# Performance work log

Hardware: AMD Instinct MI355X
Metric: run time of the kernel (lower is better)

Reference implementation:

```python
import jax, jax.numpy as jnp
import numpy as np

N = 100000
E = 1600000
IN_C = 128
OUT_C = 64
EDGE_DIM = 16
EDGE_HID = 32
EPS = 1e-5


def setup_inputs() -> dict:
    key = jax.random.key(0)
    ks = jax.random.split(key, 12)
    x = jax.random.normal(ks[0], (N, IN_C), dtype=jnp.float32)
    edge_index = jax.random.randint(ks[1], (2, E), 0, N, dtype=jnp.int64)
    edge_attr = jax.random.uniform(ks[2], (E, EDGE_DIM), dtype=jnp.float32)
    # PDNConv params
    lin_w = jax.random.normal(ks[3], (OUT_C, IN_C), dtype=jnp.float32) / np.sqrt(IN_C)
    bias = jnp.zeros((OUT_C,), dtype=jnp.float32)
    mlp_w1 = jax.random.normal(ks[4], (EDGE_HID, EDGE_DIM), dtype=jnp.float32) / np.sqrt(EDGE_DIM)
    mlp_b1 = jnp.zeros((EDGE_HID,), dtype=jnp.float32)
    mlp_w2 = jax.random.normal(ks[5], (1, EDGE_HID), dtype=jnp.float32) / np.sqrt(EDGE_HID)
    mlp_b2 = jnp.zeros((1,), dtype=jnp.float32)
    # PReLU (single shared parameter, torch default init 0.25)
    prelu_a = jnp.asarray(0.25, dtype=jnp.float32)
    # GraphNorm params
    gn_weight = jnp.ones((OUT_C,), dtype=jnp.float32)
    gn_bias = jnp.zeros((OUT_C,), dtype=jnp.float32)
    gn_mean_scale = jnp.ones((OUT_C,), dtype=jnp.float32)
    return {
        "x": x, "edge_index": edge_index, "edge_attr": edge_attr,
        "lin_w": lin_w, "bias": bias,
        "mlp_w1": mlp_w1, "mlp_b1": mlp_b1, "mlp_w2": mlp_w2, "mlp_b2": mlp_b2,
        "prelu_a": prelu_a,
        "gn_weight": gn_weight, "gn_bias": gn_bias, "gn_mean_scale": gn_mean_scale,
    }


def reference(x, edge_index, edge_attr, lin_w, bias, mlp_w1, mlp_b1, mlp_w2, mlp_b2,
              prelu_a, gn_weight, gn_bias, gn_mean_scale):
    n = x.shape[0]
    # --- PDNConv ---
    # edge MLP: Linear -> ReLU -> Linear -> Sigmoid -> scalar gate per edge
    h = jax.nn.relu(edge_attr @ mlp_w1.T + mlp_b1)           # [E, hid]
    ew = jax.nn.sigmoid(h @ mlp_w2.T + mlp_b2)[:, 0]         # [E]
    # add self-loops with weight 1.0
    loop = jnp.arange(n)
    row = jnp.concatenate([edge_index[0], loop])             # source
    col = jnp.concatenate([edge_index[1], loop])             # target
    ew = jnp.concatenate([ew, jnp.ones((n,), dtype=x.dtype)])
    # gcn_norm: D^{-1/2} A D^{-1/2} with weighted degree on targets
    deg = jax.ops.segment_sum(ew, col, num_segments=n)       # [N]
    dinv = jnp.where(deg > 0, jax.lax.rsqrt(deg), 0.0)
    norm = dinv[row] * ew * dinv[col]                        # [E+N]
    xt = x @ lin_w.T                                         # [N, out]
    msgs = norm[:, None] * xt[row]                           # gather + gate
    out = jax.ops.segment_sum(msgs, col, num_segments=n) + bias  # scatter-add
    # --- PReLU ---
    out = jnp.where(out >= 0, out, prelu_a * out)
    # --- GraphNorm (single graph) ---
    mean = out.mean(axis=0)                                  # [out]
    centered = out - gn_mean_scale * mean
    var = jnp.mean(centered * centered, axis=0)
    out = gn_weight * centered * jax.lax.rsqrt(var + EPS) + gn_bias
    return out
```

## Files before the change

kernel.cpp:

```cpp
#include <hip/hip_runtime.h>
#include <math.h>

#define IN_C   128
#define OUT_C  64
#define EDIM   16
#define EHID   32
#define GN_EPS 1e-5f

typedef unsigned long long u64;

__device__ __forceinline__ float dot4(float4 a, float4 b) {
    return a.x * b.x + a.y * b.y + a.z * b.z + a.w * b.w;
}
__device__ __forceinline__ void fma4(float4& a, float s, float4 w) {
    a.x = fmaf(s, w.x, a.x); a.y = fmaf(s, w.y, a.y);
    a.z = fmaf(s, w.z, a.z); a.w = fmaf(s, w.w, a.w);
}
__device__ __forceinline__ float getc(float4 v, int j) {
    return j == 0 ? v.x : j == 1 ? v.y : j == 2 ? v.z : v.w;
}

__global__ void k_init(u64* __restrict__ degcnt, float* __restrict__ sums, int N) {
    int i = blockIdx.x * 256 + threadIdx.x;
    if (i < N) degcnt[i] = (1ull << 32);
    if (i < 2 * OUT_C) sums[i] = 0.f;
}

__global__ void k_edge(const float* __restrict__ ea, const int* __restrict__ ei,
                       const float* __restrict__ w1, const float* __restrict__ b1,
                       const float* __restrict__ w2, const float* __restrict__ b2,
                       u64* __restrict__ degcnt, int2* __restrict__ tmp, int E) {
    __shared__ float4 sw1[EHID][4];
    __shared__ float  sb1[EHID];
    __shared__ float  sw2[EHID];
    __shared__ float  sb2;
    int tid = threadIdx.x;
    if (tid < 128) {
        const float4* w1v = (const float4*)w1;
        sw1[tid >> 2][tid & 3] = w1v[tid];
    }
    if (tid < EHID) { sb1[tid] = b1[tid]; sw2[tid] = w2[tid]; }
    if (tid == 0)   sb2 = b2[0];
    __syncthreads();

    int e = blockIdx.x * 256 + tid;
    if (e >= E) return;
    const float4* eav = (const float4*)ea + (size_t)e * 4;
    float4 a0 = eav[0], a1 = eav[1], a2 = eav[2], a3 = eav[3];
    float z = sb2;
    #pragma unroll
    for (int j = 0; j < EHID; ++j) {
        float h = dot4(a0, sw1[j][0]) + dot4(a1, sw1[j][1])
                + dot4(a2, sw1[j][2]) + dot4(a3, sw1[j][3]) + sb1[j];
        h = fmaxf(h, 0.f);
        z += h * sw2[j];
    }
    float ewv = 1.f / (1.f + __expf(-z));

    int row = ei[e];
    int col = ei[E + e];
    u64 inc = (1ull << 44) | (u64)(ewv * 4294967296.0f);
    u64 old = atomicAdd(&degcnt[col], inc);
    int rank = (int)(old >> 44);
    tmp[e] = make_int2(row | (rank << 17), __float_as_int(ewv));
}

__global__ void k_finish(const u64* __restrict__ degcnt, float* __restrict__ dinv,
                         int* __restrict__ cnt, int N) {
    int i = blockIdx.x * 256 + threadIdx.x;
    if (i < N) {
        u64 v = degcnt[i];
        float deg = (float)(v & ((1ull << 44) - 1)) * (1.f / 4294967296.f);
        dinv[i] = rsqrtf(deg);
        cnt[i] = (int)(v >> 44);
    }
}

__global__ void k_xt(const float* __restrict__ x, const float* __restrict__ lw,
                     const float* __restrict__ dinv, float* __restrict__ xts, int N) {
    __shared__ float swt[IN_C * OUT_C];
    int tid = threadIdx.x;
    for (int i = tid; i < IN_C * OUT_C; i += 256) {
        int k = i >> 6, c = i & 63;
        swt[i] = lw[c * IN_C + k];
    }
    __syncthreads();

    int lane = tid & 63;
    int c4 = lane & 15;
    int rq = lane >> 4;
    int rbase = blockIdx.x * 64 + (tid >> 6) * 16 + rq * 4;

    int r0 = min(rbase + 0, N - 1), r1 = min(rbase + 1, N - 1);
    int r2 = min(rbase + 2, N - 1), r3 = min(rbase + 3, N - 1);
    const float4* x4 = (const float4*)x;
    float4 acc0 = {0,0,0,0}, acc1 = {0,0,0,0}, acc2 = {0,0,0,0}, acc3 = {0,0,0,0};

    #pragma unroll 4
    for (int k4 = 0; k4 < IN_C / 4; ++k4) {
        float4 xv0 = x4[(size_t)r0 * 32 + k4];
        float4 xv1 = x4[(size_t)r1 * 32 + k4];
        float4 xv2 = x4[(size_t)r2 * 32 + k4];
        float4 xv3 = x4[(size_t)r3 * 32 + k4];
        #pragma unroll
        for (int j = 0; j < 4; ++j) {
            float4 wv = *(const float4*)&swt[(k4 * 4 + j) * OUT_C + (c4 << 2)];
            fma4(acc0, getc(xv0, j), wv);
            fma4(acc1, getc(xv1, j), wv);
            fma4(acc2, getc(xv2, j), wv);
            fma4(acc3, getc(xv3, j), wv);
        }
    }
    int cc = c4 << 2;
    #pragma unroll
    for (int i = 0; i < 4; ++i) {
        int r = rbase + i;
        if (r < N) {
            float d = dinv[r];
            float4 a = i == 0 ? acc0 : i == 1 ? acc1 : i == 2 ? acc2 : acc3;
            a.x *= d; a.y *= d; a.z *= d; a.w *= d;
            *(float4*)&xts[(size_t)r * OUT_C + cc] = a;
        }
    }
}

__global__ void k_scan1(const int* __restrict__ cnt, int* __restrict__ start,
                        int* __restrict__ bsums, int N) {
    __shared__ int s[256];
    int t = threadIdx.x;
    int i = blockIdx.x * 256 + t;
    int v = (i < N) ? cnt[i] : 0;
    s[t] = v;
    __syncthreads();
    #pragma unroll
    for (int off = 1; off < 256; off <<= 1) {
        int u = (t >= off) ? s[t - off] : 0;
        __syncthreads();
        s[t] += u;
        __syncthreads();
    }
    if (i < N) start[i] = s[t] - v;
    if (t == 255) bsums[blockIdx.x] = s[255];
}
__global__ void k_scan2(int* __restrict__ bsums, int nb) {
    __shared__ int s[1024];
    int t = threadIdx.x;
    s[t] = (t < nb) ? bsums[t] : 0;
    __syncthreads();
    #pragma unroll
    for (int off = 1; off < 1024; off <<= 1) {
        int u = (t >= off) ? s[t - off] : 0;
        __syncthreads();
        s[t] += u;
        __syncthreads();
    }
    if (t < nb) bsums[t] = (t == 0) ? 0 : s[t - 1];
}
__global__ void k_scan3(int* __restrict__ start, const int* __restrict__ bsums, int N) {
    int i = blockIdx.x * 256 + threadIdx.x;
    if (i < N) start[i] += bsums[blockIdx.x];
}

__global__ void k_pass2(const int* __restrict__ ei, const int2* __restrict__ tmp,
                        const int* __restrict__ start, int2* __restrict__ rec, int E) {
    int e = blockIdx.x * 256 + threadIdx.x;
    if (e >= E) return;
    int col = ei[E + e];
    int2 t = tmp[e];
    int rank = ((unsigned)t.x) >> 17;
    int pos = start[col] + rank;
    rec[pos] = make_int2(t.x & 0x1FFFF, t.y);
}

__global__ void k_gather(const int2* __restrict__ rec, const int* __restrict__ start,
                         const int* __restrict__ cnt, const float* __restrict__ dinv,
                         const float* __restrict__ xts, const float* __restrict__ bias,
                         float* __restrict__ out, int N) {
    int node = blockIdx.x * 4 + (threadIdx.x >> 6);
    if (node >= N) return;
    int lane = threadIdx.x & 63;
    int beg = start[node], num = cnt[node];
    float acc = xts[((size_t)node << 6) + lane];
    int j = 0;
    for (; j + 8 <= num; j += 8) {
        int2 rc[8];
        #pragma unroll
        for (int u = 0; u < 8; ++u) rc[u] = rec[beg + j + u];
        float v[8];
        #pragma unroll
        for (int u = 0; u < 8; ++u) v[u] = xts[((size_t)rc[u].x << 6) + lane];
        #pragma unroll
        for (int u = 0; u < 8; ++u) acc = fmaf(__int_as_float(rc[u].y), v[u], acc);
    }
    for (; j < num; ++j) {
        int2 rc = rec[beg + j];
        acc = fmaf(__int_as_float(rc.y), xts[((size_t)rc.x << 6) + lane], acc);
    }
    out[((size_t)node << 6) + lane] = bias[lane] + dinv[node] * acc;
}

__global__ void k_init_out(const float* __restrict__ bias, const float* __restrict__ dinv,
                           const float* __restrict__ xts, float* __restrict__ out, int total) {
    int t = blockIdx.x * 256 + threadIdx.x;
    if (t >= total) return;
    int i = t >> 6, c = t & 63;
    out[t] = bias[c] + dinv[i] * xts[t];
}
__global__ void k_scatter(const int* __restrict__ ei, const int2* __restrict__ tmp,
                          const float* __restrict__ dinv, const float* __restrict__ xts,
                          float* __restrict__ out, int E) {
    int t = blockIdx.x * 256 + threadIdx.x;
    int e = t >> 6;
    if (e >= E) return;
    int lane = t & 63;
    int2 tm = tmp[e];
    int row = tm.x & 0x1FFFF;
    int col = ei[E + e];
    float w = dinv[col] * __int_as_float(tm.y);
    atomicAdd(out + (size_t)col * OUT_C + lane, w * xts[(size_t)row * OUT_C + lane]);
}

__global__ void k_stats(const float* __restrict__ out, const float* __restrict__ pa,
                        float* __restrict__ sums, int total) {
    __shared__ float r1[256], r2[256];
    float a = pa[0];
    float s = 0.f, s2 = 0.f;
    int stride = gridDim.x * 256;
    for (int t = blockIdx.x * 256 + threadIdx.x; t < total; t += stride) {
        float v = out[t];
        float y = v >= 0.f ? v : a * v;
        s += y; s2 += y * y;
    }
    int tid = threadIdx.x;
    r1[tid] = s; r2[tid] = s2;
    __syncthreads();
    if (tid < 64) {
        float t1 = r1[tid] + r1[tid + 64] + r1[tid + 128] + r1[tid + 192];
        float t2 = r2[tid] + r2[tid + 64] + r2[tid + 128] + r2[tid + 192];
        atomicAdd(&sums[tid], t1);
        atomicAdd(&sums[OUT_C + tid], t2);
    }
}
__global__ void k_apply(float* __restrict__ out, const float* __restrict__ pa,
                        const float* __restrict__ sums,
                        const float* __restrict__ gw, const float* __restrict__ gb,
                        const float* __restrict__ gms, int total, float invN) {
    int t = blockIdx.x * 256 + threadIdx.x;
    if (t >= total) return;
    int c = t & 63;
    float a  = pa[0];
    float m  = sums[c] * invN;
    float ms = gms[c];
    float var = sums[OUT_C + c] * invN - ms * m * m * (2.f - ms);
    float A = gw[c] * rsqrtf(var + GN_EPS);
    float v = out[t];
    float y = v >= 0.f ? v : a * v;
    out[t] = A * (y - ms * m) + gb[c];
}

extern "C" void kernel_launch(void* const* d_in, const int* in_sizes, int n_in,
                              void* d_out, int out_size, void* d_ws, size_t ws_size,
                              hipStream_t stream) {
    (void)n_in; (void)out_size;
    const float* x    = (const float*)d_in[0];
    const int*   ei   = (const int*)  d_in[1];
    const float* ea   = (const float*)d_in[2];
    const float* lw   = (const float*)d_in[3];
    const float* bias = (const float*)d_in[4];
    const float* w1   = (const float*)d_in[5];
    const float* b1   = (const float*)d_in[6];
    const float* w2   = (const float*)d_in[7];
    const float* b2   = (const float*)d_in[8];
    const float* pa   = (const float*)d_in[9];
    const float* gw   = (const float*)d_in[10];
    const float* gb   = (const float*)d_in[11];
    const float* gms  = (const float*)d_in[12];
    float* out = (float*)d_out;

    int N = in_sizes[0] / IN_C;
    int E = in_sizes[2] / EDIM;
    int total = N * OUT_C;
    int nbN = (N + 255) / 256;
    int nbE = (E + 255) / 256;

    char* p = (char*)d_ws;
    u64*   degcnt = (u64*)p;  p += sizeof(u64) * (size_t)N;
    float* dinv   = (float*)p; p += sizeof(float) * (size_t)N;
    float* xts    = (float*)p; p += sizeof(float) * (size_t)N * OUT_C;
    float* sums   = (float*)p; p += sizeof(float) * 128;
    int*   cnt    = (int*)p;   p += sizeof(int) * (size_t)N;
    int*   startv = (int*)p;   p += sizeof(int) * (size_t)N;
    int*   bsums  = (int*)p;   p += sizeof(int) * 1024;
    int2*  tmp    = (int2*)p;  p += sizeof(int2) * (size_t)E;
    int2*  rec    = (int2*)p;  p += sizeof(int2) * (size_t)E;
    size_t need = (size_t)(p - (char*)d_ws);
    bool use_csr = (need <= ws_size) && (nbN <= 1024);

    k_init   <<<nbN, 256, 0, stream>>>(degcnt, sums, N);
    k_edge   <<<nbE, 256, 0, stream>>>(ea, ei, w1, b1, w2, b2, degcnt, tmp, E);
    k_finish <<<nbN, 256, 0, stream>>>(degcnt, dinv, cnt, N);
    k_xt     <<<(N + 63) / 64, 256, 0, stream>>>(x, lw, dinv, xts, N);

    if (use_csr) {
        k_scan1 <<<nbN, 256, 0, stream>>>(cnt, startv, bsums, N);
        k_scan2 <<<1, 1024, 0, stream>>>(bsums, nbN);
        k_scan3 <<<nbN, 256, 0, stream>>>(startv, bsums, N);
        k_pass2 <<<nbE, 256, 0, stream>>>(ei, tmp, startv, rec, E);
        k_gather<<<(N + 3) / 4, 256, 0, stream>>>(rec, startv, cnt, dinv, xts, bias, out, N);
    } else {
        k_init_out<<<(total + 255) / 256, 256, 0, stream>>>(bias, dinv, xts, out, total);
        long st = (long)E * 64;
        k_scatter <<<(unsigned)((st + 255) / 256), 256, 0, stream>>>(ei, tmp, dinv, xts, out, E);
    }

    k_stats <<<512, 256, 0, stream>>>(out, pa, sums, total);
    k_apply <<<(total + 255) / 256, 256, 0, stream>>>(out, pa, sums, gw, gb, gms, total,
                                                      1.0f / (float)N);
}
```

Measured before the change: 463.8 us.

## Compute degree from CSR segments instead of packed 64-bit atomics

Replaces the packed 64-bit atomic that accumulated fixed-point degree and rank with a 32-bit count atomic, then computes each node's weighted degree by summing its CSR segment after the scatter pass. The edge kernel now handles two edges per thread, and the scan's third pass is dropped by adding block offsets where the start array is read. The aim is cheaper atomics and fewer kernel launches. In exchange there is an extra per-node serial sweep over records and more work per thread in the edge kernel.

After: 1.504 ms. 3.24x slower.

```diff
diff --git a/kernel.cpp b/kernel.cpp
--- a/kernel.cpp
+++ b/kernel.cpp
@@ -20,60 +20,118 @@
     return j == 0 ? v.x : j == 1 ? v.y : j == 2 ? v.z : v.w;
 }
 
-__global__ void k_init(u64* __restrict__ degcnt, float* __restrict__ sums, int N) {
+__global__ void k_init(int* __restrict__ cnt, float* __restrict__ degf,
+                       float* __restrict__ sums, int N) {
     int i = blockIdx.x * 256 + threadIdx.x;
-    if (i < N) degcnt[i] = (1ull << 32);
+    if (i < N) { cnt[i] = 0; degf[i] = 0.f; }
     if (i < 2 * OUT_C) sums[i] = 0.f;
 }
 
 __global__ void k_edge(const float* __restrict__ ea, const int* __restrict__ ei,
-                       const float* __restrict__ w1, const float* __restrict__ b1,
-                       const float* __restrict__ w2, const float* __restrict__ b2,
-                       u64* __restrict__ degcnt, int2* __restrict__ tmp, int E) {
+                       const float* __restrict__ mw1, const float* __restrict__ mb1,
+                       const float* __restrict__ mw2, const float* __restrict__ mb2,
+                       int* __restrict__ cnt, int2* __restrict__ tmp, int E) {
     __shared__ float4 sw1[EHID][4];
     __shared__ float  sb1[EHID];
     __shared__ float  sw2[EHID];
     __shared__ float  sb2;
     int tid = threadIdx.x;
     if (tid < 128) {
-        const float4* w1v = (const float4*)w1;
+        const float4* w1v = (const float4*)mw1;
         sw1[tid >> 2][tid & 3] = w1v[tid];
     }
-    if (tid < EHID) { sb1[tid] = b1[tid]; sw2[tid] = w2[tid]; }
-    if (tid == 0)   sb2 = b2[0];
-    __syncthreads();
-
-    int e = blockIdx.x * 256 + tid;
-    if (e >= E) return;
-    const float4* eav = (const float4*)ea + (size_t)e * 4;
-    float4 a0 = eav[0], a1 = eav[1], a2 = eav[2], a3 = eav[3];
-    float z = sb2;
+    if (tid < EHID) { sb1[tid] = mb1[tid]; sw2[tid] = mw2[tid]; }
+    if (tid == 0)   sb2 = mb2[0];
+    __syncthreads();
+
+    int e0 = blockIdx.x * 512 + tid;
+    int e1 = e0 + 256;
+    bool v0 = e0 < E, v1 = e1 < E;
+    int e0c = min(e0, E - 1), e1c = min(e1, E - 1);
+
+    int row0 = ei[e0c], col0 = ei[E + e0c];
+    int row1 = ei[e1c], col1 = ei[E + e1c];
+    int rank0 = 0, rank1 = 0;
+    if (v0) rank0 = atomicAdd(&cnt[col0], 1);
+    if (v1) rank1 = atomicAdd(&cnt[col1], 1);
+
+    const float4* p0 = (const float4*)ea + (size_t)e0c * 4;
+    const float4* p1 = (const float4*)ea + (size_t)e1c * 4;
+    float4 a0 = p0[0], a1 = p0[1], a2 = p0[2], a3 = p0[3];
+    float4 b0 = p1[0], b1 = p1[1], b2 = p1[2], b3 = p1[3];
+
+    float z0 = sb2, z1 = sb2;
     #pragma unroll
     for (int j = 0; j < EHID; ++j) {
-        float h = dot4(a0, sw1[j][0]) + dot4(a1, sw1[j][1])
-                + dot4(a2, sw1[j][2]) + dot4(a3, sw1[j][3]) + sb1[j];
-        h = fmaxf(h, 0.f);
-        z += h * sw2[j];
-    }
-    float ewv = 1.f / (1.f + __expf(-z));
-
-    int row = ei[e];
+        float4 w0 = sw1[j][0], w1 = sw1[j][1], w2 = sw1[j][2], w3 = sw1[j][3];
+        float bj = sb1[j], wj = sw2[j];
+        float h0 = dot4(a0, w0) + dot4(a1, w1) + dot4(a2, w2) + dot4(a3, w3) + bj;
+        float h1 = dot4(b0, w0) + dot4(b1, w1) + dot4(b2, w2) + dot4(b3, w3) + bj;
+        z0 += fmaxf(h0, 0.f) * wj;
+        z1 += fmaxf(h1, 0.f) * wj;
+    }
+    float ew0 = 1.f / (1.f + __expf(-z0));
+    float ew1 = 1.f / (1.f + __expf(-z1));
+
+    if (v0) tmp[e0] = make_int2(row0 | (rank0 << 17), __float_as_int(ew0));
+    if (v1) tmp[e1] = make_int2(row1 | (rank1 << 17), __float_as_int(ew1));
+}
+
+__global__ void k_scan1(const int* __restrict__ cnt, int* __restrict__ start,
+                        int* __restrict__ bsums, int N) {
+    __shared__ int s[256];
+    int t = threadIdx.x;
+    int i = blockIdx.x * 256 + t;
+    int v = (i < N) ? cnt[i] : 0;
+    s[t] = v;
+    __syncthreads();
+    #pragma unroll
+    for (int off = 1; off < 256; off <<= 1) {
+        int u = (t >= off) ? s[t - off] : 0;
+        __syncthreads();
+        s[t] += u;
+        __syncthreads();
+    }
+    if (i < N) start[i] = s[t] - v;
+    if (t == 255) bsums[blockIdx.x] = s[255];
+}
+__global__ void k_scan2(int* __restrict__ bsums, int nb) {
+    __shared__ int s[1024];
+    int t = threadIdx.x;
+    s[t] = (t < nb) ? bsums[t] : 0;
+    __syncthreads();
+    #pragma unroll
+    for (int off = 1; off < 1024; off <<= 1) {
+        int u = (t >= off) ? s[t - off] : 0;
+        __syncthreads();
+        s[t] += u;
+        __syncthreads();
+    }
+    if (t < nb) bsums[t] = (t == 0) ? 0 : s[t - 1];
+}
+
+__global__ void k_pass2(const int* __restrict__ ei, const int2* __restrict__ tmp,
+                        const int* __restrict__ start, const int* __restrict__ bsums,
+                        int2* __restrict__ rec, int E) {
+    int e = blockIdx.x * 256 + threadIdx.x;
+    if (e >= E) return;
     int col = ei[E + e];
-    u64 inc = (1ull << 44) | (u64)(ewv * 4294967296.0f);
-    u64 old = atomicAdd(&degcnt[col], inc);
-    int rank = (int)(old >> 44);
-    tmp[e] = make_int2(row | (rank << 17), __float_as_int(ewv));
-}
-
-__global__ void k_finish(const u64* __restrict__ degcnt, float* __restrict__ dinv,
-                         int* __restrict__ cnt, int N) {
+    int2 t = tmp[e];
+    int rank = ((unsigned)t.x) >> 17;
+    int pos = start[col] + bsums[col >> 8] + rank;
+    rec[pos] = make_int2(t.x & 0x1FFFF, t.y);
+}
+
+__global__ void k_deg(const int2* __restrict__ rec, const int* __restrict__ start,
+                      const int* __restrict__ bsums, const int* __restrict__ cnt,
+                      float* __restrict__ dinv, int N) {
     int i = blockIdx.x * 256 + threadIdx.x;
-    if (i < N) {
-        u64 v = degcnt[i];
-        float deg = (float)(v & ((1ull << 44) - 1)) * (1.f / 4294967296.f);
-        dinv[i] = rsqrtf(deg);
-        cnt[i] = (int)(v >> 44);
-    }
+    if (i >= N) return;
+    int beg = start[i] + bsums[i >> 8];
+    int num = cnt[i];
+    float deg = 1.0f;
+    for (int j = 0; j < num; ++j) deg += __int_as_float(rec[beg + j].y);
+    dinv[i] = rsqrtf(deg);
 }
 
 __global__ void k_xt(const float* __restrict__ x, const float* __restrict__ lw,
@@ -124,62 +182,15 @@
     }
 }
 
-__global__ void k_scan1(const int* __restrict__ cnt, int* __restrict__ start,
-                        int* __restrict__ bsums, int N) {
-    __shared__ int s[256];
-    int t = threadIdx.x;
-    int i = blockIdx.x * 256 + t;
-    int v = (i < N) ? cnt[i] : 0;
-    s[t] = v;
-    __syncthreads();
-    #pragma unroll
-    for (int off = 1; off < 256; off <<= 1) {
-        int u = (t >= off) ? s[t - off] : 0;
-        __syncthreads();
-        s[t] += u;
-        __syncthreads();
-    }
-    if (i < N) start[i] = s[t] - v;
-    if (t == 255) bsums[blockIdx.x] = s[255];
-}
-__global__ void k_scan2(int* __restrict__ bsums, int nb) {
-    __shared__ int s[1024];
-    int t = threadIdx.x;
-    s[t] = (t < nb) ? bsums[t] : 0;
-    __syncthreads();
-    #pragma unroll
-    for (int off = 1; off < 1024; off <<= 1) {
-        int u = (t >= off) ? s[t - off] : 0;
-        __syncthreads();
-        s[t] += u;
-        __syncthreads();
-    }
-    if (t < nb) bsums[t] = (t == 0) ? 0 : s[t - 1];
-}
-__global__ void k_scan3(int* __restrict__ start, const int* __restrict__ bsums, int N) {
-    int i = blockIdx.x * 256 + threadIdx.x;
-    if (i < N) start[i] += bsums[blockIdx.x];
-}
-
-__global__ void k_pass2(const int* __restrict__ ei, const int2* __restrict__ tmp,
-                        const int* __restrict__ start, int2* __restrict__ rec, int E) {
-    int e = blockIdx.x * 256 + threadIdx.x;
-    if (e >= E) return;
-    int col = ei[E + e];
-    int2 t = tmp[e];
-    int rank = ((unsigned)t.x) >> 17;
-    int pos = start[col] + rank;
-    rec[pos] = make_int2(t.x & 0x1FFFF, t.y);
-}
-
 __global__ void k_gather(const int2* __restrict__ rec, const int* __restrict__ start,
-                         const int* __restrict__ cnt, const float* __restrict__ dinv,
-                         const float* __restrict__ xts, const float* __restrict__ bias,
-                         float* __restrict__ out, int N) {
+                         const int* __restrict__ bsums, const int* __restrict__ cnt,
+                         const float* __restrict__ dinv, const float* __restrict__ xts,
+                         const float* __restrict__ bias, float* __restrict__ out, int N) {
     int node = blockIdx.x * 4 + (threadIdx.x >> 6);
     if (node >= N) return;
     int lane = threadIdx.x & 63;
-    int beg = start[node], num = cnt[node];
+    int beg = start[node] + bsums[node >> 8];
+    int num = cnt[node];
     float acc = xts[((size_t)node << 6) + lane];
     int j = 0;
     for (; j + 8 <= num; j += 8) {
@@ -199,6 +210,16 @@
     out[((size_t)node << 6) + lane] = bias[lane] + dinv[node] * acc;
 }
 
+__global__ void k_dega(const int* __restrict__ ei, const int2* __restrict__ tmp,
+                       float* __restrict__ degf, int E) {
+    int e = blockIdx.x * 256 + threadIdx.x;
+    if (e >= E) return;
+    atomicAdd(&degf[ei[E + e]], __int_as_float(tmp[e].y));
+}
+__global__ void k_dinv(const float* __restrict__ degf, float* __restrict__ dinv, int N) {
+    int i = blockIdx.x * 256 + threadIdx.x;
+    if (i < N) dinv[i] = rsqrtf(1.f + degf[i]);
+}
 __global__ void k_init_out(const float* __restrict__ bias, const float* __restrict__ dinv,
                            const float* __restrict__ xts, float* __restrict__ out, int total) {
     int t = blockIdx.x * 256 + threadIdx.x;
@@ -282,32 +303,36 @@
     int total = N * OUT_C;
     int nbN = (N + 255) / 256;
     int nbE = (E + 255) / 256;
+    int nbE2 = (E + 511) / 512;
 
     char* p = (char*)d_ws;
-    u64*   degcnt = (u64*)p;  p += sizeof(u64) * (size_t)N;
+    float* xts    = (float*)p; p += sizeof(float) * (size_t)N * OUT_C;
+    int2*  tmp    = (int2*)p;  p += sizeof(int2) * (size_t)E;
     float* dinv   = (float*)p; p += sizeof(float) * (size_t)N;
-    float* xts    = (float*)p; p += sizeof(float) * (size_t)N * OUT_C;
     float* sums   = (float*)p; p += sizeof(float) * 128;
     int*   cnt    = (int*)p;   p += sizeof(int) * (size_t)N;
     int*   startv = (int*)p;   p += sizeof(int) * (size_t)N;
     int*   bsums  = (int*)p;   p += sizeof(int) * 1024;
-    int2*  tmp    = (int2*)p;  p += sizeof(int2) * (size_t)E;
     int2*  rec    = (int2*)p;  p += sizeof(int2) * (size_t)E;
     size_t need = (size_t)(p - (char*)d_ws);
     bool use_csr = (need <= ws_size) && (nbN <= 1024);
 
-    k_init   <<<nbN, 256, 0, stream>>>(degcnt, sums, N);
-    k_edge   <<<nbE, 256, 0, stream>>>(ea, ei, w1, b1, w2, b2, degcnt, tmp, E);
-    k_finish <<<nbN, 256, 0, stream>>>(degcnt, dinv, cnt, N);
-    k_xt     <<<(N + 63) / 64, 256, 0, stream>>>(x, lw, dinv, xts, N);
+    float* degf = (float*)startv;
+
+    k_init <<<nbN, 256, 0, stream>>>(cnt, degf, sums, N);
+    k_edge <<<nbE2, 256, 0, stream>>>(ea, ei, w1, b1, w2, b2, cnt, tmp, E);
 
     if (use_csr) {
         k_scan1 <<<nbN, 256, 0, stream>>>(cnt, startv, bsums, N);
         k_scan2 <<<1, 1024, 0, stream>>>(bsums, nbN);
-        k_scan3 <<<nbN, 256, 0, stream>>>(startv, bsums, N);
-        k_pass2 <<<nbE, 256, 0, stream>>>(ei, tmp, startv, rec, E);
-        k_gather<<<(N + 3) / 4, 256, 0, stream>>>(rec, startv, cnt, dinv, xts, bias, out, N);
+        k_pass2 <<<nbE, 256, 0, stream>>>(ei, tmp, startv, bsums, rec, E);
+        k_deg   <<<nbN, 256, 0, stream>>>(rec, startv, bsums, cnt, dinv, N);
+        k_xt    <<<(N + 63) / 64, 256, 0, stream>>>(x, lw, dinv, xts, N);
+        k_gather<<<(N + 3) / 4, 256, 0, stream>>>(rec, startv, bsums, cnt, dinv, xts, bias, out, N);
     } else {
+        k_dega  <<<nbE, 256, 0, stream>>>(ei, tmp, degf, E);
+        k_dinv  <<<nbN, 256, 0, stream>>>(degf, dinv, N);
+        k_xt    <<<(N + 63) / 64, 256, 0, stream>>>(x, lw, dinv, xts, N);
         k_init_out<<<(total + 255) / 256, 256, 0, stream>>>(bias, dinv, xts, out, total);
         long st = (long)E * 64;
         k_scatter <<<(unsigned)((st + 255) / 256), 256, 0, stream>>>(ei, tmp, dinv, xts, out, E);
```

## Fuse degree finish into scan, drop scan3, batch four edges per thread

Applied to the files above, without the earlier changes.

The degree-finish step (dinv and count) is folded into the first scan kernel. The scan3 fix-up pass is removed by adding the block offset (bsums) at the point of use in pass2 and in the gather. The edge MLP kernel now processes four edges per thread, so the shared-memory weight loads are reused across edges and more memory loads are in flight before the atomics. Together these remove two kernel launches and one full pass over the node arrays, at the cost of more registers in k_edge and an extra bsums load in pass2 and the gather.

Result: slower. 1.207 ms (+160.2%).

```diff
diff --git a/kernel.cpp b/kernel.cpp
--- a/kernel.cpp
+++ b/kernel.cpp
@@ -27,8 +27,8 @@
 }
 
 __global__ void k_edge(const float* __restrict__ ea, const int* __restrict__ ei,
-                       const float* __restrict__ w1, const float* __restrict__ b1,
-                       const float* __restrict__ w2, const float* __restrict__ b2,
+                       const float* __restrict__ mw1, const float* __restrict__ mb1,
+                       const float* __restrict__ mw2, const float* __restrict__ mb2,
                        u64* __restrict__ degcnt, int2* __restrict__ tmp, int E) {
     __shared__ float4 sw1[EHID][4];
     __shared__ float  sb1[EHID];
@@ -36,33 +36,58 @@
     __shared__ float  sb2;
     int tid = threadIdx.x;
     if (tid < 128) {
-        const float4* w1v = (const float4*)w1;
+        const float4* w1v = (const float4*)mw1;
         sw1[tid >> 2][tid & 3] = w1v[tid];
     }
-    if (tid < EHID) { sb1[tid] = b1[tid]; sw2[tid] = w2[tid]; }
-    if (tid == 0)   sb2 = b2[0];
-    __syncthreads();
-
-    int e = blockIdx.x * 256 + tid;
-    if (e >= E) return;
-    const float4* eav = (const float4*)ea + (size_t)e * 4;
-    float4 a0 = eav[0], a1 = eav[1], a2 = eav[2], a3 = eav[3];
-    float z = sb2;
+    if (tid < EHID) { sb1[tid] = mb1[tid]; sw2[tid] = mw2[tid]; }
+    if (tid == 0)   sb2 = mb2[0];
+    __syncthreads();
+
+    int base = blockIdx.x * 1024 + tid;
+
+    float4 A[4][4];
+    int row[4], col[4];
+    #pragma unroll
+    for (int q = 0; q < 4; ++q) {
+        int e  = base + q * 256;
+        int ec = min(e, E - 1);
+        row[q] = ei[ec];
+        col[q] = ei[E + ec];
+        const float4* p = (const float4*)ea + (size_t)ec * 4;
+        A[q][0] = p[0]; A[q][1] = p[1]; A[q][2] = p[2]; A[q][3] = p[3];
+    }
+
+    float z[4] = {sb2, sb2, sb2, sb2};
     #pragma unroll
     for (int j = 0; j < EHID; ++j) {
-        float h = dot4(a0, sw1[j][0]) + dot4(a1, sw1[j][1])
-                + dot4(a2, sw1[j][2]) + dot4(a3, sw1[j][3]) + sb1[j];
-        h = fmaxf(h, 0.f);
-        z += h * sw2[j];
-    }
-    float ewv = 1.f / (1.f + __expf(-z));
-
-    int row = ei[e];
-    int col = ei[E + e];
-    u64 inc = (1ull << 44) | (u64)(ewv * 4294967296.0f);
-    u64 old = atomicAdd(&degcnt[col], inc);
-    int rank = (int)(old >> 44);
-    tmp[e] = make_int2(row | (rank << 17), __float_as_int(ewv));
+        float4 w0 = sw1[j][0], w1 = sw1[j][1], w2 = sw1[j][2], w3 = sw1[j][3];
+        float bj = sb1[j], wj = sw2[j];
+        #pragma unroll
+        for (int q = 0; q < 4; ++q) {
+            float h = dot4(A[q][0], w0) + dot4(A[q][1], w1)
+                    + dot4(A[q][2], w2) + dot4(A[q][3], w3) + bj;
+            z[q] += fmaxf(h, 0.f) * wj;
+        }
+    }
+
+    float ewv[4];
+    u64 old[4];
+    #pragma unroll
+    for (int q = 0; q < 4; ++q) {
+        ewv[q] = 1.f / (1.f + __expf(-z[q]));
+        if (base + q * 256 < E) {
+            u64 inc = (1ull << 44) | (u64)(ewv[q] * 4294967296.0f);
+            old[q] = atomicAdd(&degcnt[col[q]], inc);
+        }
+    }
+    #pragma unroll
+    for (int q = 0; q < 4; ++q) {
+        int e = base + q * 256;
+        if (e < E) {
+            int rank = (int)(old[q] >> 44);
+            tmp[e] = make_int2(row[q] | (rank << 17), __float_as_int(ewv[q]));
+        }
+    }
 }
 
 __global__ void k_finish(const u64* __restrict__ degcnt, float* __restrict__ dinv,
@@ -76,6 +101,59 @@
     }
 }
 
+__global__ void k_scan1(const u64* __restrict__ degcnt, int* __restrict__ start,
+                        int* __restrict__ bsums, float* __restrict__ dinv,
+                        int* __restrict__ cnt, int N) {
+    __shared__ int s[256];
+    int t = threadIdx.x;
+    int i = blockIdx.x * 256 + t;
+    int v = 0;
+    if (i < N) {
+        u64 dv = degcnt[i];
+        v = (int)(dv >> 44);
+        float deg = (float)(dv & ((1ull << 44) - 1)) * (1.f / 4294967296.f);
+        dinv[i] = rsqrtf(deg);
+        cnt[i] = v;
+    }
+    s[t] = v;
+    __syncthreads();
+    #pragma unroll
+    for (int off = 1; off < 256; off <<= 1) {
+        int u = (t >= off) ? s[t - off] : 0;
+        __syncthreads();
+        s[t] += u;
+        __syncthreads();
+    }
+    if (i < N) start[i] = s[t] - v;
+    if (t == 255) bsums[blockIdx.x] = s[255];
+}
+__global__ void k_scan2(int* __restrict__ bsums, int nb) {
+    __shared__ int s[1024];
+    int t = threadIdx.x;
+    s[t] = (t < nb) ? bsums[t] : 0;
+    __syncthreads();
+    #pragma unroll
+    for (int off = 1; off < 1024; off <<= 1) {
+        int u = (t >= off) ? s[t - off] : 0;
+        __syncthreads();
+        s[t] += u;
+        __syncthreads();
+    }
+    if (t < nb) bsums[t] = (t == 0) ? 0 : s[t - 1];
+}
+
+__global__ void k_pass2(const int* __restrict__ ei, const int2* __restrict__ tmp,
+                        const int* __restrict__ start, const int* __restrict__ bsums,
+                        int2* __restrict__ rec, int E) {
+    int e = blockIdx.x * 256 + threadIdx.x;
+    if (e >= E) return;
+    int col = ei[E + e];
+    int2 t = tmp[e];
+    int rank = ((unsigned)t.x) >> 17;
+    int pos = start[col] + bsums[col >> 8] + rank;
+    rec[pos] = make_int2(t.x & 0x1FFFF, t.y);
+}
+
 __global__ void k_xt(const float* __restrict__ x, const float* __restrict__ lw,
                      const float* __restrict__ dinv, float* __restrict__ xts, int N) {
     __shared__ float swt[IN_C * OUT_C];
@@ -124,62 +202,15 @@
     }
 }
 
-__global__ void k_scan1(const int* __restrict__ cnt, int* __restrict__ start,
-                        int* __restrict__ bsums, int N) {
-    __shared__ int s[256];
-    int t = threadIdx.x;
-    int i = blockIdx.x * 256 + t;
-    int v = (i < N) ? cnt[i] : 0;
-    s[t] = v;
-    __syncthreads();
-    #pragma unroll
-    for (int off = 1; off < 256; off <<= 1) {
-        int u = (t >= off) ? s[t - off] : 0;
-        __syncthreads();
-        s[t] += u;
-        __syncthreads();
-    }
-    if (i < N) start[i] = s[t] - v;
-    if (t == 255) bsums[blockIdx.x] = s[255];
-}
-__global__ void k_scan2(int* __restrict__ bsums, int nb) {
-    __shared__ int s[1024];
-    int t = threadIdx.x;
-    s[t] = (t < nb) ? bsums[t] : 0;
-    __syncthreads();
-    #pragma unroll
-    for (int off = 1; off < 1024; off <<= 1) {
-        int u = (t >= off) ? s[t - off] : 0;
-        __syncthreads();
-        s[t] += u;
-        __syncthreads();
-    }
-    if (t < nb) bsums[t] = (t == 0) ? 0 : s[t - 1];
-}
-__global__ void k_scan3(int* __restrict__ start, const int* __restrict__ bsums, int N) {
-    int i = blockIdx.x * 256 + threadIdx.x;
-    if (i < N) start[i] += bsums[blockIdx.x];
-}
-
-__global__ void k_pass2(const int* __restrict__ ei, const int2* __restrict__ tmp,
-                        const int* __restrict__ start, int2* __restrict__ rec, int E) {
-    int e = blockIdx.x * 256 + threadIdx.x;
-    if (e >= E) return;
-    int col = ei[E + e];
-    int2 t = tmp[e];
-    int rank = ((unsigned)t.x) >> 17;
-    int pos = start[col] + rank;
-    rec[pos] = make_int2(t.x & 0x1FFFF, t.y);
-}
-
 __global__ void k_gather(const int2* __restrict__ rec, const int* __restrict__ start,
-                         const int* __restrict__ cnt, const float* __restrict__ dinv,
-                         const float* __restrict__ xts, const float* __restrict__ bias,
-                         float* __restrict__ out, int N) {
+                         const int* __restrict__ bsums, const int* __restrict__ cnt,
+                         const float* __restrict__ dinv, const float* __restrict__ xts,
+                         const float* __restrict__ bias, float* __restrict__ out, int N) {
     int node = blockIdx.x * 4 + (threadIdx.x >> 6);
     if (node >= N) return;
     int lane = threadIdx.x & 63;
-    int beg = start[node], num = cnt[node];
+    int beg = start[node] + bsums[node >> 8];
+    int num = cnt[node];
     float acc = xts[((size_t)node << 6) + lane];
     int j = 0;
     for (; j + 8 <= num; j += 8) {
@@ -282,6 +313,7 @@
     int total = N * OUT_C;
     int nbN = (N + 255) / 256;
     int nbE = (E + 255) / 256;
+    int nbE4 = (E + 1023) / 1024;
 
     char* p = (char*)d_ws;
     u64*   degcnt = (u64*)p;  p += sizeof(u64) * (size_t)N;
@@ -296,18 +328,18 @@
     size_t need = (size_t)(p - (char*)d_ws);
     bool use_csr = (need <= ws_size) && (nbN <= 1024);
 
-    k_init   <<<nbN, 256, 0, stream>>>(degcnt, sums, N);
-    k_edge   <<<nbE, 256, 0, stream>>>(ea, ei, w1, b1, w2, b2, degcnt, tmp, E);
-    k_finish <<<nbN, 256, 0, stream>>>(degcnt, dinv, cnt, N);
-    k_xt     <<<(N + 63) / 64, 256, 0, stream>>>(x, lw, dinv, xts, N);
+    k_init <<<nbN, 256, 0, stream>>>(degcnt, sums, N);
+    k_edge <<<nbE4, 256, 0, stream>>>(ea, ei, w1, b1, w2, b2, degcnt, tmp, E);
 
     if (use_csr) {
-        k_scan1 <<<nbN, 256, 0, stream>>>(cnt, startv, bsums, N);
+        k_scan1 <<<nbN, 256, 0, stream>>>(degcnt, startv, bsums, dinv, cnt, N);
         k_scan2 <<<1, 1024, 0, stream>>>(bsums, nbN);
-        k_scan3 <<<nbN, 256, 0, stream>>>(startv, bsums, N);
-        k_pass2 <<<nbE, 256, 0, stream>>>(ei, tmp, startv, rec, E);
-        k_gather<<<(N + 3) / 4, 256, 0, stream>>>(rec, startv, cnt, dinv, xts, bias, out, N);
+        k_pass2 <<<nbE, 256, 0, stream>>>(ei, tmp, startv, bsums, rec, E);
+        k_xt    <<<(N + 63) / 64, 256, 0, stream>>>(x, lw, dinv, xts, N);
+        k_gather<<<(N + 3) / 4, 256, 0, stream>>>(rec, startv, bsums, cnt, dinv, xts, bias, out, N);
     } else {
+        k_finish<<<nbN, 256, 0, stream>>>(degcnt, dinv, cnt, N);
+        k_xt    <<<(N + 63) / 64, 256, 0, stream>>>(x, lw, dinv, xts, N);
         k_init_out<<<(total + 255) / 256, 256, 0, stream>>>(bias, dinv, xts, out, total);
         long st = (long)E * 64;
         k_scatter <<<(unsigned)((st + 255) / 256), 256, 0, stream>>>(ei, tmp, dinv, xts, out, E);
```
